# Performance work log

Measured on AMD Instinct MI355X. Metric: run time of the kernel, lower is better.

## Reference

```python
import jax, jax.numpy as jnp
import numpy as np

BATCH, SEQ, D, N = 4, 2048, 768, 16
S_A = -0.5


def setup_inputs() -> dict:
    key = jax.random.key(0)
    ks = jax.random.split(key, 6)
    u = jax.random.normal(ks[0], (BATCH, SEQ, D), dtype=jnp.float32)
    # A = -10*rand + s_A, with first state of every channel pinned to s_A (init-time op)
    A = S_A - 10.0 * jax.random.uniform(ks[1], (D, N), dtype=jnp.float32)
    A = A.at[:, 0].set(S_A)
    W_B = jax.random.normal(ks[2], (N, D), dtype=jnp.float32)
    W_C = jax.random.normal(ks[3], (N, D), dtype=jnp.float32)
    q_delta = jax.random.normal(ks[4], (D,), dtype=jnp.float32)
    p_delta = jax.random.normal(ks[5], (1,), dtype=jnp.float32)
    return {"u": u, "A": A, "W_B": W_B, "W_C": W_C, "q_delta": q_delta, "p_delta": p_delta}


def reference(u, A, W_B, W_C, q_delta, p_delta):
    # delta = softplus(p_delta + u @ q_delta)  -> (b, l)
    delta = jax.nn.softplus(p_delta[0] + jnp.einsum('bld,d->bl', u, q_delta))
    # input-dependent B, C projections: (b, l, n)
    B = jnp.einsum('nd,bld->bln', W_B, u)
    C = jnp.einsum('nd,bld->bln', W_C, u)
    # discretize: (b, l, d, n)
    deltaA = jnp.exp(delta[..., None, None] * A)
    deltaB_u = delta[..., None, None] * u[..., :, None] * B[:, :, None, :]

    def step(x, inp):
        dA_t, dBu_t, C_t = inp          # (b,d,n), (b,d,n), (b,n)
        x = dA_t * x + dBu_t            # (b,d,n)
        y = jnp.einsum('bdn,bn->bd', x, C_t)
        return x, y

    x0 = jnp.zeros((u.shape[0], A.shape[0], A.shape[1]), dtype=u.dtype)
    xs = (jnp.moveaxis(deltaA, 1, 0), jnp.moveaxis(deltaB_u, 1, 0), jnp.moveaxis(C, 1, 0))
    _, ys = jax.lax.scan(step, x0, xs)  # ys: (l, b, d)
    return jnp.moveaxis(ys, 0, 1)       # (b, l, d)
```

## Files before the change

### kernel.cpp

```cpp
#include <hip/hip_runtime.h>
#include <math.h>


#define BATCH 4
#define SEQ   2048
#define DDIM  768
#define NST   16
#define CHUNK 64
#define NC    (SEQ / CHUNK)
#define ROWS  (BATCH * SEQ)
#define DT    (DDIM / 128)
#define NOUT  33
#define LOG2E 1.4426950408889634f
#define FIX_THR 64.0f

__device__ __forceinline__ float fexp2(float x) {
#if __has_builtin(__builtin_amdgcn_exp2f)
  return __builtin_amdgcn_exp2f(x);
#else
  return exp2f(x);
#endif
}

__global__ __launch_bounds__(256) void k_proj(
    const float* __restrict__ u, const float* __restrict__ W_B,
    const float* __restrict__ W_C, const float* __restrict__ q_delta,
    const float* __restrict__ p_delta, float* __restrict__ delta,
    float* __restrict__ Bm, float* __restrict__ Cm) {
  __shared__ float Ws[NOUT * 128];
  __shared__ float Ps[4][16][NOUT];

  const int tid  = threadIdx.x;
  const int rloc = tid & 15;
  const int ks   = tid >> 4;
  const int row  = blockIdx.x * 16 + rloc;

  float acc[NOUT];
#pragma unroll
  for (int j = 0; j < NOUT; ++j) acc[j] = 0.0f;

  const float* up0 = u + (size_t)row * DDIM + ks * 8;

  for (int kt = 0; kt < 6; ++kt) {
    for (int f4 = tid; f4 < NOUT * 32; f4 += 256) {
      const int j   = f4 >> 5;
      const int rem = f4 & 31;
      const float* base = (j < 16) ? (W_B + j * DDIM)
                        : (j < 32) ? (W_C + (j - 16) * DDIM)
                                   : q_delta;
      ((float4*)Ws)[f4] = ((const float4*)(base + kt * 128))[rem];
    }
    __syncthreads();

    const float* up = up0 + kt * 128;
    const float4 a0 = ((const float4*)up)[0];
    const float4 a1 = ((const float4*)up)[1];
#pragma unroll
    for (int j = 0; j < NOUT; ++j) {
      const float4* wp = (const float4*)(Ws + j * 128 + ks * 8);
      const float4 w0 = wp[0], w1 = wp[1];
      float s = acc[j];
      s = fmaf(a0.x, w0.x, s); s = fmaf(a0.y, w0.y, s);
      s = fmaf(a0.z, w0.z, s); s = fmaf(a0.w, w0.w, s);
      s = fmaf(a1.x, w1.x, s); s = fmaf(a1.y, w1.y, s);
      s = fmaf(a1.z, w1.z, s); s = fmaf(a1.w, w1.w, s);
      acc[j] = s;
    }
    __syncthreads();
  }

  const int wave = tid >> 6;
#pragma unroll
  for (int j = 0; j < NOUT; ++j) {
    acc[j] += __shfl_xor(acc[j], 16);
    acc[j] += __shfl_xor(acc[j], 32);
  }
  if ((tid & 48) == 0) {
#pragma unroll
    for (int j = 0; j < NOUT; ++j) Ps[wave][rloc][j] = acc[j];
  }
  __syncthreads();

  for (int f = tid; f < 16 * NOUT; f += 256) {
    const int r = f / NOUT, j = f - r * NOUT;
    const float s = Ps[0][r][j] + Ps[1][r][j] + Ps[2][r][j] + Ps[3][r][j];
    const int grow = blockIdx.x * 16 + r;
    if (j < 16) {
      Bm[grow * NST + j] = s;
    } else if (j < 32) {
      Cm[grow * NST + (j - 16)] = s;
    } else {
      const float z = p_delta[0] + s;
      delta[grow] = fmaxf(z, 0.0f) + log1pf(expf(-fabsf(z)));
    }
  }
}

__global__ __launch_bounds__(256) void k_scan(
    const float* __restrict__ u, const float* __restrict__ A,
    const float* __restrict__ delta, const float* __restrict__ Bm,
    const float* __restrict__ Cm, float* __restrict__ y,
    float* __restrict__ xend) {
  __shared__ float sdelta[CHUNK];
  __shared__ float Bs[CHUNK * NST];
  __shared__ float Cs[CHUNK * NST];

  const int dt  = blockIdx.x % DT;
  const int c   = (blockIdx.x / DT) % NC;
  const int b   = blockIdx.x / (DT * NC);
  const int tid = threadIdx.x;
  const int h   = tid & 1;
  const int dl  = tid >> 1;
  const int d   = dt * 128 + dl;
  const int r0  = b * SEQ + c * CHUNK;

  for (int i = tid; i < CHUNK * NST; i += 256) {
    Bs[i] = Bm[r0 * NST + i];
    Cs[i] = Cm[r0 * NST + i];
  }
  if (tid < CHUNK) sdelta[tid] = delta[r0 + tid];
  __syncthreads();

  float A2[8];
  {
    const float4* ap = (const float4*)(A + d * NST + h * 8);
    const float4 t0 = ap[0], t1 = ap[1];
    A2[0] = t0.x * LOG2E; A2[1] = t0.y * LOG2E;
    A2[2] = t0.z * LOG2E; A2[3] = t0.w * LOG2E;
    A2[4] = t1.x * LOG2E; A2[5] = t1.y * LOG2E;
    A2[6] = t1.z * LOG2E; A2[7] = t1.w * LOG2E;
  }
  float x[8];
#pragma unroll
  for (int n = 0; n < 8; ++n) x[n] = 0.0f;

  const float* up = u + (size_t)r0 * DDIM + d;
  float*       yp = y + (size_t)r0 * DDIM + d;

  for (int i = 0; i < CHUNK; ++i) {
    const float dlt = sdelta[i];
    const float du  = dlt * up[(size_t)i * DDIM];

    const float4* Bp = (const float4*)(Bs + i * NST + h * 8);
    const float4* Cp = (const float4*)(Cs + i * NST + h * 8);
    const float4 b0 = Bp[0], b1 = Bp[1];
    const float4 c0 = Cp[0], c1 = Cp[1];
    const float bv[8] = {b0.x, b0.y, b0.z, b0.w, b1.x, b1.y, b1.z, b1.w};
    const float cv[8] = {c0.x, c0.y, c0.z, c0.w, c1.x, c1.y, c1.z, c1.w};

    float a0 = 0.0f, a1 = 0.0f;
#pragma unroll
    for (int n = 0; n < 8; ++n) {
      const float e = fexp2(A2[n] * dlt);
      x[n] = fmaf(e, x[n], du * bv[n]);
      if (n < 4) a0 = fmaf(x[n], cv[n], a0);
      else       a1 = fmaf(x[n], cv[n], a1);
    }
    float ys = a0 + a1;
    ys += __shfl_xor(ys, 1);
    if (h == 0) yp[(size_t)i * DDIM] = ys;
  }

  float4* xe =
      (float4*)(xend + ((size_t)((b * NC + c) * DDIM + d)) * NST + h * 8);
  xe[0] = make_float4(x[0], x[1], x[2], x[3]);
  xe[1] = make_float4(x[4], x[5], x[6], x[7]);
}

__global__ __launch_bounds__(256) void k_carry(
    const float* __restrict__ A, const float* __restrict__ delta,
    float* __restrict__ xend) {
  __shared__ float Ds[NC];
  const int b    = blockIdx.x / (DDIM / 16);
  const int dblk = blockIdx.x % (DDIM / 16);
  const int tid  = threadIdx.x;

  {
    float s = 0.0f;
    const float* dp = delta + b * SEQ + tid * 8;
#pragma unroll
    for (int k = 0; k < 8; ++k) s += dp[k];
    s += __shfl_xor(s, 1);
    s += __shfl_xor(s, 2);
    s += __shfl_xor(s, 4);
    if ((tid & 7) == 0) Ds[tid >> 3] = s;
  }
  __syncthreads();

  const int n = tid & 15;
  const int d = dblk * 16 + (tid >> 4);
  const float A2 = A[d * NST + n] * LOG2E;

  float carry = 0.0f;
  for (int c = 0; c < NC; ++c) {
    const size_t idx = ((size_t)((b * NC + c) * DDIM + d)) * NST + n;
    const float xe = xend[idx];
    const float P  = fexp2(A2 * Ds[c]);
    xend[idx] = carry;
    carry = fmaf(P, carry, xe);
  }
}

__global__ __launch_bounds__(256) void k_fix(
    const float* __restrict__ A, const float* __restrict__ delta,
    const float* __restrict__ Cm, const float* __restrict__ xend,
    float* __restrict__ y) {
  __shared__ float sdelta[CHUNK];
  const int dt  = blockIdx.x % DT;
  const int c   = (blockIdx.x / DT) % (NC - 1) + 1;
  const int b   = blockIdx.x / (DT * (NC - 1));
  const int tid = threadIdx.x;
  const int h   = tid & 1;
  const int dl  = tid >> 1;
  const int d   = dt * 128 + dl;
  const int r0  = b * SEQ + c * CHUNK;

  if (tid < CHUNK) sdelta[tid] = delta[r0 + tid];
  __syncthreads();

  float A2[8], carry[8];
  {
    const float4* ap = (const float4*)(A + d * NST + h * 8);
    const float4 t0 = ap[0], t1 = ap[1];
    A2[0] = t0.x * LOG2E; A2[1] = t0.y * LOG2E;
    A2[2] = t0.z * LOG2E; A2[3] = t0.w * LOG2E;
    A2[4] = t1.x * LOG2E; A2[5] = t1.y * LOG2E;
    A2[6] = t1.z * LOG2E; A2[7] = t1.w * LOG2E;
    const float4* cp = (const float4*)(
        xend + ((size_t)((b * NC + c) * DDIM + d)) * NST + h * 8);
    const float4 q0 = cp[0], q1 = cp[1];
    carry[0] = q0.x; carry[1] = q0.y; carry[2] = q0.z; carry[3] = q0.w;
    carry[4] = q1.x; carry[5] = q1.y; carry[6] = q1.z; carry[7] = q1.w;
  }

  const float* Cp0 = Cm + (size_t)r0 * NST + h * 8;
  float* yp = y + (size_t)r0 * DDIM + d;

  float dS = 0.0f;
  for (int i = 0; i < CHUNK; ++i) {
    dS += sdelta[i];
    if (dS > FIX_THR) break;
    const float4* Cp = (const float4*)(Cp0 + i * NST);
    const float4 c0 = Cp[0], c1 = Cp[1];
    const float cv[8] = {c0.x, c0.y, c0.z, c0.w, c1.x, c1.y, c1.z, c1.w};
    float a0 = 0.0f, a1 = 0.0f;
#pragma unroll
    for (int n = 0; n < 8; ++n) {
      const float e = fexp2(A2[n] * dS);
      if (n < 4) a0 = fmaf(e * carry[n], cv[n], a0);
      else       a1 = fmaf(e * carry[n], cv[n], a1);
    }
    float ys = a0 + a1;
    ys += __shfl_xor(ys, 1);
    if (h == 0) yp[(size_t)i * DDIM] += ys;
  }
}

extern "C" void kernel_launch(void* const* d_in, const int* in_sizes, int n_in,
                              void* d_out, int out_size, void* d_ws,
                              size_t ws_size, hipStream_t stream) {
  const float* u       = (const float*)d_in[0];
  const float* A       = (const float*)d_in[1];
  const float* W_B     = (const float*)d_in[2];
  const float* W_C     = (const float*)d_in[3];
  const float* q_delta = (const float*)d_in[4];
  const float* p_delta = (const float*)d_in[5];
  float* y  = (float*)d_out;
  float* ws = (float*)d_ws;

  float* delta = ws;
  float* Bm    = ws + 8192;
  float* Cm    = ws + 139264;
  float* xend  = ws + 270336;

  hipLaunchKernelGGL(k_proj, dim3(ROWS / 16), dim3(256), 0, stream,
                     u, W_B, W_C, q_delta, p_delta, delta, Bm, Cm);
  hipLaunchKernelGGL(k_scan, dim3(BATCH * NC * DT), dim3(256), 0, stream,
                     u, A, delta, Bm, Cm, y, xend);
  hipLaunchKernelGGL(k_carry, dim3(BATCH * (DDIM / 16)), dim3(256), 0, stream,
                     A, delta, xend);
  hipLaunchKernelGGL(k_fix, dim3(BATCH * (NC - 1) * DT), dim3(256), 0, stream,
                     A, delta, Cm, xend, y);
}
```

Measured before the change: 145.7 us.

## Restructure projection GEMM, prefetch u in scan, fold carry pass into fix kernel

The projection kernel is rewritten so each block handles 8 rows. Weights are read straight from global memory into registers, u tiles are double-buffered in shared memory, and the K reduction moves to wave shuffles instead of a shared-memory partial-sum array. The scan kernel prefetches the next u element one step ahead. The separate carry-propagation kernel is removed: each fix block now rebuilds its incoming state by walking backward over the earlier chunk end-states, stopping once the cumulative decay passes the threshold. This saves a launch and a serial pass, but adds redundant per-block work and extra barriers inside the backward loop.

```diff
diff --git a/kernel.cpp b/kernel.cpp
--- a/kernel.cpp
+++ b/kernel.cpp
@@ -10,7 +10,6 @@
 #define NC    (SEQ / CHUNK)
 #define ROWS  (BATCH * SEQ)
 #define DT    (DDIM / 128)
-#define NOUT  33
 #define LOG2E 1.4426950408889634f
 #define FIX_THR 64.0f
 
@@ -27,71 +26,107 @@
     const float* __restrict__ W_C, const float* __restrict__ q_delta,
     const float* __restrict__ p_delta, float* __restrict__ delta,
     float* __restrict__ Bm, float* __restrict__ Cm) {
-  __shared__ float Ws[NOUT * 128];
-  __shared__ float Ps[4][16][NOUT];
-
-  const int tid  = threadIdx.x;
-  const int rloc = tid & 15;
-  const int ks   = tid >> 4;
-  const int row  = blockIdx.x * 16 + rloc;
-
-  float acc[NOUT];
-#pragma unroll
-  for (int j = 0; j < NOUT; ++j) acc[j] = 0.0f;
-
-  const float* up0 = u + (size_t)row * DDIM + ks * 8;
+  __shared__ float u_s[2][8 * 128];
+
+  const int tid = threadIdx.x;
+  const int jg  = tid >> 5;
+  const int ks  = tid & 31;
+  const int r0  = blockIdx.x * 8;
+
+  const float* wrow[4];
+#pragma unroll
+  for (int jj = 0; jj < 4; ++jj) {
+    const int j = jg * 4 + jj;
+    wrow[jj] = (j < 16) ? (W_B + (size_t)j * DDIM)
+                        : (W_C + (size_t)(j - 16) * DDIM);
+  }
+
+  const float* ubase = u + (size_t)r0 * DDIM;
+  ((float4*)u_s[0])[tid] =
+      *(const float4*)(ubase + (size_t)(tid >> 5) * DDIM + (tid & 31) * 4);
+
+  float acc[4][8];
+#pragma unroll
+  for (int jj = 0; jj < 4; ++jj)
+#pragma unroll
+    for (int r = 0; r < 8; ++r) acc[jj][r] = 0.0f;
+  float accd[8];
+#pragma unroll
+  for (int r = 0; r < 8; ++r) accd[r] = 0.0f;
 
   for (int kt = 0; kt < 6; ++kt) {
-    for (int f4 = tid; f4 < NOUT * 32; f4 += 256) {
-      const int j   = f4 >> 5;
-      const int rem = f4 & 31;
-      const float* base = (j < 16) ? (W_B + j * DDIM)
-                        : (j < 32) ? (W_C + (j - 16) * DDIM)
-                                   : q_delta;
-      ((float4*)Ws)[f4] = ((const float4*)(base + kt * 128))[rem];
-    }
     __syncthreads();
-
-    const float* up = up0 + kt * 128;
-    const float4 a0 = ((const float4*)up)[0];
-    const float4 a1 = ((const float4*)up)[1];
-#pragma unroll
-    for (int j = 0; j < NOUT; ++j) {
-      const float4* wp = (const float4*)(Ws + j * 128 + ks * 8);
-      const float4 w0 = wp[0], w1 = wp[1];
-      float s = acc[j];
-      s = fmaf(a0.x, w0.x, s); s = fmaf(a0.y, w0.y, s);
-      s = fmaf(a0.z, w0.z, s); s = fmaf(a0.w, w0.w, s);
-      s = fmaf(a1.x, w1.x, s); s = fmaf(a1.y, w1.y, s);
-      s = fmaf(a1.z, w1.z, s); s = fmaf(a1.w, w1.w, s);
-      acc[j] = s;
-    }
-    __syncthreads();
-  }
-
-  const int wave = tid >> 6;
-#pragma unroll
-  for (int j = 0; j < NOUT; ++j) {
-    acc[j] += __shfl_xor(acc[j], 16);
-    acc[j] += __shfl_xor(acc[j], 32);
-  }
-  if ((tid & 48) == 0) {
-#pragma unroll
-    for (int j = 0; j < NOUT; ++j) Ps[wave][rloc][j] = acc[j];
-  }
-  __syncthreads();
-
-  for (int f = tid; f < 16 * NOUT; f += 256) {
-    const int r = f / NOUT, j = f - r * NOUT;
-    const float s = Ps[0][r][j] + Ps[1][r][j] + Ps[2][r][j] + Ps[3][r][j];
-    const int grow = blockIdx.x * 16 + r;
-    if (j < 16) {
-      Bm[grow * NST + j] = s;
-    } else if (j < 32) {
-      Cm[grow * NST + (j - 16)] = s;
-    } else {
-      const float z = p_delta[0] + s;
-      delta[grow] = fmaxf(z, 0.0f) + log1pf(expf(-fabsf(z)));
+    float4 nxt;
+    if (kt < 5)
+      nxt = *(const float4*)(ubase + (size_t)(tid >> 5) * DDIM +
+                             (kt + 1) * 128 + (tid & 31) * 4);
+    float4 w[4];
+#pragma unroll
+    for (int jj = 0; jj < 4; ++jj)
+      w[jj] = *(const float4*)(wrow[jj] + kt * 128 + ks * 4);
+    float4 qd = make_float4(0.f, 0.f, 0.f, 0.f);
+    if (jg == 0) qd = *(const float4*)(q_delta + kt * 128 + ks * 4);
+
+    const float4* us = (const float4*)u_s[kt & 1];
+#pragma unroll
+    for (int r = 0; r < 8; ++r) {
+      const float4 uv = us[r * 32 + ks];
+#pragma unroll
+      for (int jj = 0; jj < 4; ++jj) {
+        float s = acc[jj][r];
+        s = fmaf(uv.x, w[jj].x, s); s = fmaf(uv.y, w[jj].y, s);
+        s = fmaf(uv.z, w[jj].z, s); s = fmaf(uv.w, w[jj].w, s);
+        acc[jj][r] = s;
+      }
+      if (jg == 0) {
+        float s = accd[r];
+        s = fmaf(uv.x, qd.x, s); s = fmaf(uv.y, qd.y, s);
+        s = fmaf(uv.z, qd.z, s); s = fmaf(uv.w, qd.w, s);
+        accd[r] = s;
+      }
+    }
+    if (kt < 5) ((float4*)u_s[(kt + 1) & 1])[tid] = nxt;
+  }
+
+#pragma unroll
+  for (int jj = 0; jj < 4; ++jj)
+#pragma unroll
+    for (int r = 0; r < 8; ++r) {
+      float s = acc[jj][r];
+      s += __shfl_xor(s, 1);  s += __shfl_xor(s, 2);
+      s += __shfl_xor(s, 4);  s += __shfl_xor(s, 8);
+      s += __shfl_xor(s, 16);
+      acc[jj][r] = s;
+    }
+  if (jg == 0) {
+#pragma unroll
+    for (int r = 0; r < 8; ++r) {
+      float s = accd[r];
+      s += __shfl_xor(s, 1);  s += __shfl_xor(s, 2);
+      s += __shfl_xor(s, 4);  s += __shfl_xor(s, 8);
+      s += __shfl_xor(s, 16);
+      accd[r] = s;
+    }
+  }
+
+  if (ks == 0) {
+#pragma unroll
+    for (int jj = 0; jj < 4; ++jj) {
+      const int j = jg * 4 + jj;
+#pragma unroll
+      for (int r = 0; r < 8; ++r) {
+        const int row = r0 + r;
+        if (j < 16) Bm[row * NST + j] = acc[jj][r];
+        else        Cm[row * NST + (j - 16)] = acc[jj][r];
+      }
+    }
+    if (jg == 0) {
+      const float p = p_delta[0];
+#pragma unroll
+      for (int r = 0; r < 8; ++r) {
+        const float z = p + accd[r];
+        delta[r0 + r] = fmaxf(z, 0.0f) + log1pf(expf(-fabsf(z)));
+      }
     }
   }
 }
@@ -137,9 +172,13 @@
   const float* up = u + (size_t)r0 * DDIM + d;
   float*       yp = y + (size_t)r0 * DDIM + d;
 
+  float u_nxt = up[0];
   for (int i = 0; i < CHUNK; ++i) {
+    const float u_cur = u_nxt;
+    if (i + 1 < CHUNK) u_nxt = up[(size_t)(i + 1) * DDIM];
+
     const float dlt = sdelta[i];
-    const float du  = dlt * up[(size_t)i * DDIM];
+    const float du  = dlt * u_cur;
 
     const float4* Bp = (const float4*)(Bs + i * NST + h * 8);
     const float4* Cp = (const float4*)(Cs + i * NST + h * 8);
@@ -167,45 +206,12 @@
   xe[1] = make_float4(x[4], x[5], x[6], x[7]);
 }
 
-__global__ __launch_bounds__(256) void k_carry(
-    const float* __restrict__ A, const float* __restrict__ delta,
-    float* __restrict__ xend) {
-  __shared__ float Ds[NC];
-  const int b    = blockIdx.x / (DDIM / 16);
-  const int dblk = blockIdx.x % (DDIM / 16);
-  const int tid  = threadIdx.x;
-
-  {
-    float s = 0.0f;
-    const float* dp = delta + b * SEQ + tid * 8;
-#pragma unroll
-    for (int k = 0; k < 8; ++k) s += dp[k];
-    s += __shfl_xor(s, 1);
-    s += __shfl_xor(s, 2);
-    s += __shfl_xor(s, 4);
-    if ((tid & 7) == 0) Ds[tid >> 3] = s;
-  }
-  __syncthreads();
-
-  const int n = tid & 15;
-  const int d = dblk * 16 + (tid >> 4);
-  const float A2 = A[d * NST + n] * LOG2E;
-
-  float carry = 0.0f;
-  for (int c = 0; c < NC; ++c) {
-    const size_t idx = ((size_t)((b * NC + c) * DDIM + d)) * NST + n;
-    const float xe = xend[idx];
-    const float P  = fexp2(A2 * Ds[c]);
-    xend[idx] = carry;
-    carry = fmaf(P, carry, xe);
-  }
-}
-
 __global__ __launch_bounds__(256) void k_fix(
     const float* __restrict__ A, const float* __restrict__ delta,
     const float* __restrict__ Cm, const float* __restrict__ xend,
     float* __restrict__ y) {
   __shared__ float sdelta[CHUNK];
+  __shared__ float sDs;
   const int dt  = blockIdx.x % DT;
   const int c   = (blockIdx.x / DT) % (NC - 1) + 1;
   const int b   = blockIdx.x / (DT * (NC - 1));
@@ -216,9 +222,8 @@
   const int r0  = b * SEQ + c * CHUNK;
 
   if (tid < CHUNK) sdelta[tid] = delta[r0 + tid];
-  __syncthreads();
-
-  float A2[8], carry[8];
+
+  float A2[8];
   {
     const float4* ap = (const float4*)(A + d * NST + h * 8);
     const float4 t0 = ap[0], t1 = ap[1];
@@ -226,11 +231,38 @@
     A2[2] = t0.z * LOG2E; A2[3] = t0.w * LOG2E;
     A2[4] = t1.x * LOG2E; A2[5] = t1.y * LOG2E;
     A2[6] = t1.z * LOG2E; A2[7] = t1.w * LOG2E;
+  }
+
+  float carry[8]  = {0.f, 0.f, 0.f, 0.f, 0.f, 0.f, 0.f, 0.f};
+  float factor[8] = {1.f, 1.f, 1.f, 1.f, 1.f, 1.f, 1.f, 1.f};
+  float cumD = 0.0f;
+  for (int cb = c - 1; cb >= 0; --cb) {
     const float4* cp = (const float4*)(
-        xend + ((size_t)((b * NC + c) * DDIM + d)) * NST + h * 8);
+        xend + ((size_t)((b * NC + cb) * DDIM + d)) * NST + h * 8);
     const float4 q0 = cp[0], q1 = cp[1];
-    carry[0] = q0.x; carry[1] = q0.y; carry[2] = q0.z; carry[3] = q0.w;
-    carry[4] = q1.x; carry[5] = q1.y; carry[6] = q1.z; carry[7] = q1.w;
+    carry[0] = fmaf(factor[0], q0.x, carry[0]);
+    carry[1] = fmaf(factor[1], q0.y, carry[1]);
+    carry[2] = fmaf(factor[2], q0.z, carry[2]);
+    carry[3] = fmaf(factor[3], q0.w, carry[3]);
+    carry[4] = fmaf(factor[4], q1.x, carry[4]);
+    carry[5] = fmaf(factor[5], q1.y, carry[5]);
+    carry[6] = fmaf(factor[6], q1.z, carry[6]);
+    carry[7] = fmaf(factor[7], q1.w, carry[7]);
+
+    __syncthreads();
+    if (tid < 64) {
+      float v = delta[b * SEQ + cb * CHUNK + tid];
+      v += __shfl_xor(v, 1);  v += __shfl_xor(v, 2);
+      v += __shfl_xor(v, 4);  v += __shfl_xor(v, 8);
+      v += __shfl_xor(v, 16); v += __shfl_xor(v, 32);
+      if (tid == 0) sDs = v;
+    }
+    __syncthreads();
+    const float Ds = sDs;
+    cumD += Ds;
+    if (cumD > FIX_THR) break;
+#pragma unroll
+    for (int n = 0; n < 8; ++n) factor[n] *= fexp2(A2[n] * Ds);
   }
 
   const float* Cp0 = Cm + (size_t)r0 * NST + h * 8;
@@ -273,12 +305,10 @@
   float* Cm    = ws + 139264;
   float* xend  = ws + 270336;
 
-  hipLaunchKernelGGL(k_proj, dim3(ROWS / 16), dim3(256), 0, stream,
+  hipLaunchKernelGGL(k_proj, dim3(ROWS / 8), dim3(256), 0, stream,
                      u, W_B, W_C, q_delta, p_delta, delta, Bm, Cm);
   hipLaunchKernelGGL(k_scan, dim3(BATCH * NC * DT), dim3(256), 0, stream,
                      u, A, delta, Bm, Cm, y, xend);
-  hipLaunchKernelGGL(k_carry, dim3(BATCH * (DDIM / 16)), dim3(256), 0, stream,
-                     A, delta, xend);
   hipLaunchKernelGGL(k_fix, dim3(BATCH * (NC - 1) * DT), dim3(256), 0, stream,
                      A, delta, Cm, xend, y);
 }
```

Measured after the change: 141.1 us. -3.2%, faster.
